# Kernel optimization log

Measured on AMD Instinct MI355X. Metric: run time of the kernel, lower is better.

## Reference

```python
import jax, jax.numpy as jnp
import numpy as np

ALPHA = 0.2  # leaky-relu negative slope AND the residual scale self.alpha

def setup_inputs() -> dict:
    key = jax.random.key(0)
    k1, k2, k3 = jax.random.split(key, 3)
    B, N, C_in, C_out = 8, 2048, 128, 128
    text = jax.random.normal(k1, (B, N, C_in), dtype=jnp.float32)
    adj = jnp.ones((B, N, N), dtype=jnp.float32)  # unused by the layer's forward
    W = jax.random.normal(k2, (C_in, C_out), dtype=jnp.float32) * (1.414 / np.sqrt(C_in + C_out))
    a = jax.random.normal(k3, (2 * C_out, 1), dtype=jnp.float32) * (1.414 / np.sqrt(2 * C_out + 1))
    return {"text": text, "adj": adj, "W": W, "a": a}

def reference(text, adj, W, a):
    # text: [B,N,C_in]; adj is unused (faithful to the source forward).
    h = jnp.einsum('bnc,cf->bnf', text, W)                  # [B,N,F]
    F_out = W.shape[1]
    a1 = a[:F_out, 0]                                       # score contribution of node i
    a2 = a[F_out:, 0]                                       # score contribution of node j
    s1 = jnp.einsum('bnf,f->bn', h, a1)                     # [B,N]
    s2 = jnp.einsum('bnf,f->bn', h, a2)                     # [B,N]
    # leakyrelu(cat(h_i,h_j) @ a) == leakyrelu(s1_i + s2_j): avoids O(N^2*2F) concat
    e = jax.nn.leaky_relu(s1[:, :, None] + s2[:, None, :], negative_slope=ALPHA)  # [B,N,N]
    attention = jax.nn.softmax(e, axis=2)                   # dropout is a no-op in eval mode
    h_prime = jnp.einsum('bij,bjf->bif', attention, h)      # [B,N,F]
    return jax.nn.elu(h_prime + ALPHA * h)
```

## Files before the change

kernel.cpp:

```cpp
#include <hip/hip_runtime.h>
#include <math.h>

#define LRELU_ALPHA 0.2f

constexpr int B_ = 8;
constexpr int N_ = 2048;
constexpr int C_ = 128;
constexpr int M_ = B_ * N_;
constexpr int SEG = 64;
constexpr int NSEG = N_ / SEG;

__global__ __launch_bounds__(512) void k_gemm(const float* __restrict__ text,
                                              const float* __restrict__ W,
                                              float* __restrict__ h) {
    __shared__ float As[64 * 33];
    __shared__ float Ws[32 * 128];
    const int tid = threadIdx.x;
    const int r0  = blockIdx.x * 64;
    const int cx  = tid & 15;
    const int ry  = tid >> 4;
    const int c0  = cx * 8;
    const int rr0 = ry * 2;

    float acc[2][8];
#pragma unroll
    for (int i = 0; i < 2; ++i)
#pragma unroll
        for (int j = 0; j < 8; ++j) acc[i][j] = 0.f;

    for (int kk = 0; kk < 128; kk += 32) {
        for (int idx = tid; idx < 64 * 32; idx += 512) {
            int r = idx >> 5, c = idx & 31;
            As[r * 33 + c] = text[(r0 + r) * 128 + kk + c];
        }
        for (int idx = tid; idx < 32 * 128; idx += 512) {
            int k = idx >> 7, f = idx & 127;
            Ws[k * 128 + f] = W[(kk + k) * 128 + f];
        }
        __syncthreads();
#pragma unroll
        for (int k = 0; k < 32; ++k) {
            float4 w0 = *(const float4*)&Ws[k * 128 + c0];
            float4 w1 = *(const float4*)&Ws[k * 128 + c0 + 4];
#pragma unroll
            for (int i = 0; i < 2; ++i) {
                float av = As[(rr0 + i) * 33 + k];
                acc[i][0] += av * w0.x; acc[i][1] += av * w0.y;
                acc[i][2] += av * w0.z; acc[i][3] += av * w0.w;
                acc[i][4] += av * w1.x; acc[i][5] += av * w1.y;
                acc[i][6] += av * w1.z; acc[i][7] += av * w1.w;
            }
        }
        __syncthreads();
    }
#pragma unroll
    for (int i = 0; i < 2; ++i) {
        int row = r0 + rr0 + i;
        float4 o0 = {acc[i][0], acc[i][1], acc[i][2], acc[i][3]};
        float4 o1 = {acc[i][4], acc[i][5], acc[i][6], acc[i][7]};
        *(float4*)&h[row * 128 + c0]     = o0;
        *(float4*)&h[row * 128 + c0 + 4] = o1;
    }
}

__global__ __launch_bounds__(256) void k_s12(const float* __restrict__ h,
                                             const float* __restrict__ a,
                                             float* __restrict__ s1,
                                             float* __restrict__ s2) {
    const int row = blockIdx.x * 4 + (threadIdx.x >> 6);
    const int t   = threadIdx.x & 63;
    float v0 = h[row * 128 + t];
    float v1 = h[row * 128 + 64 + t];
    float p1 = v0 * a[t]       + v1 * a[64 + t];
    float p2 = v0 * a[128 + t] + v1 * a[192 + t];
#pragma unroll
    for (int off = 32; off >= 1; off >>= 1) {
        p1 += __shfl_xor(p1, off);
        p2 += __shfl_xor(p2, off);
    }
    if (t == 0) { s1[row] = p1; s2[row] = p2; }
}

__global__ __launch_bounds__(1024) void k_sortscan(const float* __restrict__ s2,
                                                   float* __restrict__ s2s,
                                                   int* __restrict__ perm,
                                                   float* __restrict__ eN,
                                                   float* __restrict__ eP,
                                                   float* __restrict__ PreZ,
                                                   float* __restrict__ SufZ) {
    __shared__ float key[2048];
    __shared__ int   idxv[2048];
    __shared__ float arrN[2048];
    __shared__ float arrP[2048];
    const int b = blockIdx.x;
    const int tid = threadIdx.x;

    for (int t = tid; t < 2048; t += 1024) { key[t] = s2[b * 2048 + t]; idxv[t] = t; }
    __syncthreads();

    for (int k = 2; k <= 2048; k <<= 1) {
        for (int j = k >> 1; j > 0; j >>= 1) {
            for (int t = tid; t < 2048; t += 1024) {
                int ixj = t ^ j;
                if (ixj > t) {
                    bool up = ((t & k) == 0);
                    float ka = key[t], kb = key[ixj];
                    if ((ka > kb) == up) {
                        key[t] = kb; key[ixj] = ka;
                        int tmp = idxv[t]; idxv[t] = idxv[ixj]; idxv[ixj] = tmp;
                    }
                }
            }
            __syncthreads();
        }
    }

    for (int t = tid; t < 2048; t += 1024) {
        float kv = key[t];
        float en = expf(LRELU_ALPHA * kv);
        float ep = expf(kv);
        arrN[t] = en;
        s2s[b * 2048 + t] = kv;
        perm[b * 2048 + t] = idxv[t];
        eN[b * 2048 + t] = en;
        eP[b * 2048 + t] = ep;
    }
    __syncthreads();
    for (int t = tid; t < 2048; t += 1024) arrP[t] = expf(key[2047 - t]);
    __syncthreads();

    for (int off = 1; off < 2048; off <<= 1) {
        int t0 = tid, t1 = tid + 1024;
        float n0 = (t0 >= off) ? arrN[t0 - off] : 0.f;
        float n1 = (t1 >= off) ? arrN[t1 - off] : 0.f;
        float p0 = (t0 >= off) ? arrP[t0 - off] : 0.f;
        float p1 = (t1 >= off) ? arrP[t1 - off] : 0.f;
        __syncthreads();
        arrN[t0] += n0; arrN[t1] += n1;
        arrP[t0] += p0; arrP[t1] += p1;
        __syncthreads();
    }

    for (int t = tid; t < 2048; t += 1024) {
        PreZ[b * 2049 + t + 1] = arrN[t];
        SufZ[b * 2049 + t]     = arrP[2047 - t];
    }
    if (tid == 0) { PreZ[b * 2049] = 0.f; SufZ[b * 2049 + 2048] = 0.f; }
}

__global__ __launch_bounds__(128) void k_segsum(const float* __restrict__ h,
                                                const int* __restrict__ perm,
                                                const float* __restrict__ eN,
                                                const float* __restrict__ eP,
                                                float* __restrict__ segN,
                                                float* __restrict__ segP) {
    const int blk = blockIdx.x;
    const int b = blk >> 5, s = blk & 31;
    const int f = threadIdx.x;
    const int rbase = s * SEG;
    float an = 0.f, ap = 0.f;
    for (int r = 0; r < SEG; ++r) {
        int rr = b * 2048 + rbase + r;
        float hv = h[(b * 2048 + perm[rr]) * 128 + f];
        an += eN[rr] * hv;
        ap += eP[rr] * hv;
    }
    segN[blk * 128 + f] = an;
    segP[blk * 128 + f] = ap;
}

__global__ __launch_bounds__(128) void k_segoff(const float* __restrict__ segN,
                                                const float* __restrict__ segP,
                                                float* __restrict__ offN,
                                                float* __restrict__ offP) {
    const int b = blockIdx.x;
    const int f = threadIdx.x;
    float an = 0.f;
    for (int s = 0; s < NSEG; ++s) {
        int o = (b * NSEG + s) * 128 + f;
        offN[o] = an; an += segN[o];
    }
    float ap = 0.f;
    for (int s = NSEG - 1; s >= 0; --s) {
        int o = (b * NSEG + s) * 128 + f;
        offP[o] = ap; ap += segP[o];
    }
}

__global__ __launch_bounds__(128) void k_prefix(const float* __restrict__ h,
                                                const int* __restrict__ perm,
                                                const float* __restrict__ eN,
                                                const float* __restrict__ eP,
                                                const float* __restrict__ offN,
                                                const float* __restrict__ offP,
                                                float* __restrict__ Pre,
                                                float* __restrict__ Suf) {
    const int blk = blockIdx.x;
    const int b = blk >> 5, s = blk & 31;
    const int f = threadIdx.x;
    const int rbase = s * SEG;

    float hv[SEG];
    float an = offN[blk * 128 + f];
#pragma unroll
    for (int r = 0; r < SEG; ++r) {
        int rr = b * 2048 + rbase + r;
        hv[r] = h[(b * 2048 + perm[rr]) * 128 + f];
        Pre[(b * 2049 + rbase + r) * 128 + f] = an;
        an += eN[rr] * hv[r];
    }
    float ap = offP[blk * 128 + f];
#pragma unroll
    for (int r = SEG - 1; r >= 0; --r) {
        int rr = b * 2048 + rbase + r;
        ap += eP[rr] * hv[r];
        Suf[(b * 2049 + rbase + r) * 128 + f] = ap;
    }
    if (s == NSEG - 1) {
        Pre[(b * 2049 + 2048) * 128 + f] = an;
        Suf[(b * 2049 + 2048) * 128 + f] = 0.f;
    }
}

__global__ __launch_bounds__(256) void k_out(const float* __restrict__ h,
                                             const float* __restrict__ s1,
                                             const float* __restrict__ s2s,
                                             const float* __restrict__ PreZ,
                                             const float* __restrict__ SufZ,
                                             const float* __restrict__ Pre,
                                             const float* __restrict__ Suf,
                                             float* __restrict__ out) {
    const int tid = threadIdx.x;
    const int lr = tid >> 7, f = tid & 127;
    const int i = blockIdx.x * 2 + lr;
    const int b = i >> 11;

    const float s1v = s1[i];
    const float thr = -s1v;
    const float* keys = s2s + b * 2048;
    int lo = 0, hi = 2048;
    while (lo < hi) {
        int mid = (lo + hi) >> 1;
        if (keys[mid] <= thr) lo = mid + 1; else hi = mid;
    }
    const int r = lo;

    const float E1 = expf(s1v);
    const float E2 = expf(LRELU_ALPHA * s1v);
    const float Z  = E1 * SufZ[b * 2049 + r] + E2 * PreZ[b * 2049 + r];
    const int o = (b * 2049 + r) * 128 + f;
    const float hp = (E1 * Suf[o] + E2 * Pre[o]) / Z;
    const float hvv = h[i * 128 + f];
    const float x = hp + LRELU_ALPHA * hvv;
    out[i * 128 + f] = (x > 0.f) ? x : expm1f(x);
}

extern "C" void kernel_launch(void* const* d_in, const int* in_sizes, int n_in,
                              void* d_out, int out_size, void* d_ws, size_t ws_size,
                              hipStream_t stream) {
    const float* text = (const float*)d_in[0];
    const float* W = (const float*)d_in[2];
    const float* a = (const float*)d_in[3];
    float* out = (float*)d_out;

    float* p = (float*)d_ws;
    float* h    = p; p += (size_t)M_ * 128;
    float* s1   = p; p += M_;
    float* s2   = p; p += M_;
    float* s2s  = p; p += M_;
    int*   perm = (int*)p; p += M_;
    float* eN   = p; p += M_;
    float* eP   = p; p += M_;
    float* PreZ = p; p += B_ * 2049;
    float* SufZ = p; p += B_ * 2049;
    float* segN = p; p += B_ * NSEG * 128;
    float* segP = p; p += B_ * NSEG * 128;
    float* offN = p; p += B_ * NSEG * 128;
    float* offP = p; p += B_ * NSEG * 128;
    float* Pre  = p; p += (size_t)B_ * 2049 * 128;
    float* Suf  = p; p += (size_t)B_ * 2049 * 128;

    hipLaunchKernelGGL(k_gemm,     dim3(M_ / 64),   dim3(512),  0, stream, text, W, h);
    hipLaunchKernelGGL(k_s12,      dim3(M_ / 4),    dim3(256),  0, stream, h, a, s1, s2);
    hipLaunchKernelGGL(k_sortscan, dim3(B_),        dim3(1024), 0, stream, s2, s2s, perm, eN, eP, PreZ, SufZ);
    hipLaunchKernelGGL(k_segsum,   dim3(B_ * NSEG), dim3(128),  0, stream, h, perm, eN, eP, segN, segP);
    hipLaunchKernelGGL(k_segoff,   dim3(B_),        dim3(128),  0, stream, segN, segP, offN, offP);
    hipLaunchKernelGGL(k_prefix,   dim3(B_ * NSEG), dim3(128),  0, stream, h, perm, eN, eP, offN, offP, Pre, Suf);
    hipLaunchKernelGGL(k_out,      dim3(M_ / 2),    dim3(256),  0, stream, h, s1, s2s, PreZ, SufZ, Pre, Suf, out);
}
```

Before: 264.2 us.

## Replace bitonic sort with parallel rank counting and fuse score projection into GEMM

Fuses the s1/s2 projection and the exp computations into the GEMM epilogue. The single-block-per-batch bitonic sort and scan become a brute-force rank kernel spread over 256 blocks: each node counts how many keys are smaller to find its sorted position, and computes its threshold count and partition sums directly. This removes the binary search in the output kernel. It also halves the segment size and drops the segment-offset kernel by having each prefix block sum earlier segment totals itself. The aim is to remove the serial, low-occupancy sort stage and two kernel launches, at the cost of O(N^2) comparisons per batch and redundant offset sums.

```diff
diff --git a/kernel.cpp b/kernel.cpp
--- a/kernel.cpp
+++ b/kernel.cpp
@@ -5,14 +5,18 @@
 
 constexpr int B_ = 8;
 constexpr int N_ = 2048;
-constexpr int C_ = 128;
 constexpr int M_ = B_ * N_;
-constexpr int SEG = 64;
+constexpr int SEG = 32;
 constexpr int NSEG = N_ / SEG;
 
 __global__ __launch_bounds__(512) void k_gemm(const float* __restrict__ text,
                                               const float* __restrict__ W,
-                                              float* __restrict__ h) {
+                                              const float* __restrict__ a,
+                                              float* __restrict__ h,
+                                              float* __restrict__ s1,
+                                              float* __restrict__ s2,
+                                              float* __restrict__ eN0,
+                                              float* __restrict__ eP0) {
     __shared__ float As[64 * 33];
     __shared__ float Ws[32 * 128];
     const int tid = threadIdx.x;
@@ -53,6 +57,12 @@
         }
         __syncthreads();
     }
+
+    float4 a10 = *(const float4*)&a[c0];
+    float4 a11 = *(const float4*)&a[c0 + 4];
+    float4 a20 = *(const float4*)&a[128 + c0];
+    float4 a21 = *(const float4*)&a[128 + c0 + 4];
+
 #pragma unroll
     for (int i = 0; i < 2; ++i) {
         int row = r0 + rr0 + i;
@@ -60,160 +70,151 @@
         float4 o1 = {acc[i][4], acc[i][5], acc[i][6], acc[i][7]};
         *(float4*)&h[row * 128 + c0]     = o0;
         *(float4*)&h[row * 128 + c0 + 4] = o1;
-    }
-}
-
-__global__ __launch_bounds__(256) void k_s12(const float* __restrict__ h,
-                                             const float* __restrict__ a,
-                                             float* __restrict__ s1,
-                                             float* __restrict__ s2) {
-    const int row = blockIdx.x * 4 + (threadIdx.x >> 6);
-    const int t   = threadIdx.x & 63;
-    float v0 = h[row * 128 + t];
-    float v1 = h[row * 128 + 64 + t];
-    float p1 = v0 * a[t]       + v1 * a[64 + t];
-    float p2 = v0 * a[128 + t] + v1 * a[192 + t];
-#pragma unroll
-    for (int off = 32; off >= 1; off >>= 1) {
-        p1 += __shfl_xor(p1, off);
-        p2 += __shfl_xor(p2, off);
-    }
-    if (t == 0) { s1[row] = p1; s2[row] = p2; }
-}
-
-__global__ __launch_bounds__(1024) void k_sortscan(const float* __restrict__ s2,
-                                                   float* __restrict__ s2s,
-                                                   int* __restrict__ perm,
-                                                   float* __restrict__ eN,
-                                                   float* __restrict__ eP,
-                                                   float* __restrict__ PreZ,
-                                                   float* __restrict__ SufZ) {
-    __shared__ float key[2048];
-    __shared__ int   idxv[2048];
-    __shared__ float arrN[2048];
-    __shared__ float arrP[2048];
-    const int b = blockIdx.x;
+
+        float p1 = o0.x * a10.x + o0.y * a10.y + o0.z * a10.z + o0.w * a10.w
+                 + o1.x * a11.x + o1.y * a11.y + o1.z * a11.z + o1.w * a11.w;
+        float p2 = o0.x * a20.x + o0.y * a20.y + o0.z * a20.z + o0.w * a20.w
+                 + o1.x * a21.x + o1.y * a21.y + o1.z * a21.z + o1.w * a21.w;
+#pragma unroll
+        for (int off = 8; off >= 1; off >>= 1) {
+            p1 += __shfl_xor(p1, off);
+            p2 += __shfl_xor(p2, off);
+        }
+        if (cx == 0) {
+            s1[row] = p1;
+            s2[row] = p2;
+            eN0[row] = expf(LRELU_ALPHA * p2);
+            eP0[row] = expf(p2);
+        }
+    }
+}
+
+__global__ __launch_bounds__(512) void k_rank(const float* __restrict__ s2,
+                                              const float* __restrict__ eN0,
+                                              const float* __restrict__ eP0,
+                                              const float* __restrict__ s1,
+                                              int* __restrict__ perm,
+                                              float* __restrict__ eNs,
+                                              float* __restrict__ ePs,
+                                              int* __restrict__ rank,
+                                              float* __restrict__ ZN,
+                                              float* __restrict__ ZP) {
+    __shared__ float ls2[2048], leN[2048], leP[2048];
+    __shared__ int   redc[512], redm[512];
+    __shared__ float redn[512], redp[512];
+
+    const int b  = blockIdx.x >> 5;
+    const int eb = blockIdx.x & 31;
     const int tid = threadIdx.x;
-
-    for (int t = tid; t < 2048; t += 1024) { key[t] = s2[b * 2048 + t]; idxv[t] = t; }
+    const int e = tid & 63;
+    const int c = tid >> 6;
+
+    {
+        const float4* g2 = (const float4*)(s2  + b * 2048);
+        const float4* gn = (const float4*)(eN0 + b * 2048);
+        const float4* gp = (const float4*)(eP0 + b * 2048);
+        ((float4*)ls2)[tid] = g2[tid];
+        ((float4*)leN)[tid] = gn[tid];
+        ((float4*)leP)[tid] = gp[tid];
+    }
     __syncthreads();
 
-    for (int k = 2; k <= 2048; k <<= 1) {
-        for (int j = k >> 1; j > 0; j >>= 1) {
-            for (int t = tid; t < 2048; t += 1024) {
-                int ixj = t ^ j;
-                if (ixj > t) {
-                    bool up = ((t & k) == 0);
-                    float ka = key[t], kb = key[ixj];
-                    if ((ka > kb) == up) {
-                        key[t] = kb; key[ixj] = ka;
-                        int tmp = idxv[t]; idxv[t] = idxv[ixj]; idxv[ixj] = tmp;
-                    }
-                }
-            }
-            __syncthreads();
-        }
-    }
-
-    for (int t = tid; t < 2048; t += 1024) {
-        float kv = key[t];
-        float en = expf(LRELU_ALPHA * kv);
-        float ep = expf(kv);
-        arrN[t] = en;
-        s2s[b * 2048 + t] = kv;
-        perm[b * 2048 + t] = idxv[t];
-        eN[b * 2048 + t] = en;
-        eP[b * 2048 + t] = ep;
-    }
+    const int i  = eb * 64 + e;
+    const int gi = b * 2048 + i;
+    const float myS2 = ls2[i];
+    const float thr  = -s1[gi];
+
+    int cnt = 0, mr = 0;
+    float sn = 0.f, sp = 0.f;
+    const int j0 = c * 256;
+#pragma unroll 4
+    for (int j = j0; j < j0 + 256; j += 4) {
+        float4 v  = *(const float4*)&ls2[j];
+        float4 en = *(const float4*)&leN[j];
+        float4 ep = *(const float4*)&leP[j];
+#define PROC(vv, ee, pp, jj)                                             \
+        { bool le = (vv) <= thr;                                         \
+          cnt += le ? 1 : 0;                                             \
+          sn  += le ? (ee) : 0.f;                                        \
+          sp  += le ? 0.f : (pp);                                        \
+          mr  += ((vv) < myS2 || ((vv) == myS2 && (jj) < i)) ? 1 : 0; }
+        PROC(v.x, en.x, ep.x, j + 0)
+        PROC(v.y, en.y, ep.y, j + 1)
+        PROC(v.z, en.z, ep.z, j + 2)
+        PROC(v.w, en.w, ep.w, j + 3)
+#undef PROC
+    }
+    redc[tid] = cnt; redm[tid] = mr; redn[tid] = sn; redp[tid] = sp;
     __syncthreads();
-    for (int t = tid; t < 2048; t += 1024) arrP[t] = expf(key[2047 - t]);
-    __syncthreads();
-
-    for (int off = 1; off < 2048; off <<= 1) {
-        int t0 = tid, t1 = tid + 1024;
-        float n0 = (t0 >= off) ? arrN[t0 - off] : 0.f;
-        float n1 = (t1 >= off) ? arrN[t1 - off] : 0.f;
-        float p0 = (t0 >= off) ? arrP[t0 - off] : 0.f;
-        float p1 = (t1 >= off) ? arrP[t1 - off] : 0.f;
-        __syncthreads();
-        arrN[t0] += n0; arrN[t1] += n1;
-        arrP[t0] += p0; arrP[t1] += p1;
-        __syncthreads();
-    }
-
-    for (int t = tid; t < 2048; t += 1024) {
-        PreZ[b * 2049 + t + 1] = arrN[t];
-        SufZ[b * 2049 + t]     = arrP[2047 - t];
-    }
-    if (tid == 0) { PreZ[b * 2049] = 0.f; SufZ[b * 2049 + 2048] = 0.f; }
+    if (c == 0) {
+        int tc = 0, tm = 0; float tn = 0.f, tp = 0.f;
+#pragma unroll
+        for (int cc = 0; cc < 8; ++cc) {
+            tc += redc[cc * 64 + e];
+            tm += redm[cc * 64 + e];
+            tn += redn[cc * 64 + e];
+            tp += redp[cc * 64 + e];
+        }
+        perm[b * 2048 + tm] = i;
+        eNs [b * 2048 + tm] = leN[i];
+        ePs [b * 2048 + tm] = leP[i];
+        rank[gi] = tc;
+        ZN[gi] = tn;
+        ZP[gi] = tp;
+    }
 }
 
 __global__ __launch_bounds__(128) void k_segsum(const float* __restrict__ h,
                                                 const int* __restrict__ perm,
-                                                const float* __restrict__ eN,
-                                                const float* __restrict__ eP,
+                                                const float* __restrict__ eNs,
+                                                const float* __restrict__ ePs,
                                                 float* __restrict__ segN,
                                                 float* __restrict__ segP) {
     const int blk = blockIdx.x;
-    const int b = blk >> 5, s = blk & 31;
+    const int b = blk >> 6, s = blk & 63;
     const int f = threadIdx.x;
     const int rbase = s * SEG;
     float an = 0.f, ap = 0.f;
+#pragma unroll 4
     for (int r = 0; r < SEG; ++r) {
         int rr = b * 2048 + rbase + r;
         float hv = h[(b * 2048 + perm[rr]) * 128 + f];
-        an += eN[rr] * hv;
-        ap += eP[rr] * hv;
+        an += eNs[rr] * hv;
+        ap += ePs[rr] * hv;
     }
     segN[blk * 128 + f] = an;
     segP[blk * 128 + f] = ap;
 }
 
-__global__ __launch_bounds__(128) void k_segoff(const float* __restrict__ segN,
-                                                const float* __restrict__ segP,
-                                                float* __restrict__ offN,
-                                                float* __restrict__ offP) {
-    const int b = blockIdx.x;
-    const int f = threadIdx.x;
-    float an = 0.f;
-    for (int s = 0; s < NSEG; ++s) {
-        int o = (b * NSEG + s) * 128 + f;
-        offN[o] = an; an += segN[o];
-    }
-    float ap = 0.f;
-    for (int s = NSEG - 1; s >= 0; --s) {
-        int o = (b * NSEG + s) * 128 + f;
-        offP[o] = ap; ap += segP[o];
-    }
-}
-
 __global__ __launch_bounds__(128) void k_prefix(const float* __restrict__ h,
                                                 const int* __restrict__ perm,
-                                                const float* __restrict__ eN,
-                                                const float* __restrict__ eP,
-                                                const float* __restrict__ offN,
-                                                const float* __restrict__ offP,
+                                                const float* __restrict__ eNs,
+                                                const float* __restrict__ ePs,
+                                                const float* __restrict__ segN,
+                                                const float* __restrict__ segP,
                                                 float* __restrict__ Pre,
                                                 float* __restrict__ Suf) {
     const int blk = blockIdx.x;
-    const int b = blk >> 5, s = blk & 31;
+    const int b = blk >> 6, s = blk & 63;
     const int f = threadIdx.x;
     const int rbase = s * SEG;
 
+    float an = 0.f, ap = 0.f;
+    for (int ss = 0; ss < s; ++ss)        an += segN[(b * NSEG + ss) * 128 + f];
+    for (int ss = s + 1; ss < NSEG; ++ss) ap += segP[(b * NSEG + ss) * 128 + f];
+
     float hv[SEG];
-    float an = offN[blk * 128 + f];
 #pragma unroll
     for (int r = 0; r < SEG; ++r) {
         int rr = b * 2048 + rbase + r;
         hv[r] = h[(b * 2048 + perm[rr]) * 128 + f];
         Pre[(b * 2049 + rbase + r) * 128 + f] = an;
-        an += eN[rr] * hv[r];
-    }
-    float ap = offP[blk * 128 + f];
+        an += eNs[rr] * hv[r];
+    }
 #pragma unroll
     for (int r = SEG - 1; r >= 0; --r) {
         int rr = b * 2048 + rbase + r;
-        ap += eP[rr] * hv[r];
+        ap += ePs[rr] * hv[r];
         Suf[(b * 2049 + rbase + r) * 128 + f] = ap;
     }
     if (s == NSEG - 1) {
@@ -224,9 +225,9 @@
 
 __global__ __launch_bounds__(256) void k_out(const float* __restrict__ h,
                                              const float* __restrict__ s1,
-                                             const float* __restrict__ s2s,
-                                             const float* __restrict__ PreZ,
-                                             const float* __restrict__ SufZ,
+                                             const int* __restrict__ rank,
+                                             const float* __restrict__ ZN,
+                                             const float* __restrict__ ZP,
                                              const float* __restrict__ Pre,
                                              const float* __restrict__ Suf,
                                              float* __restrict__ out) {
@@ -236,22 +237,13 @@
     const int b = i >> 11;
 
     const float s1v = s1[i];
-    const float thr = -s1v;
-    const float* keys = s2s + b * 2048;
-    int lo = 0, hi = 2048;
-    while (lo < hi) {
-        int mid = (lo + hi) >> 1;
-        if (keys[mid] <= thr) lo = mid + 1; else hi = mid;
-    }
-    const int r = lo;
-
     const float E1 = expf(s1v);
     const float E2 = expf(LRELU_ALPHA * s1v);
-    const float Z  = E1 * SufZ[b * 2049 + r] + E2 * PreZ[b * 2049 + r];
+    const int   r  = rank[i];
+    const float Z  = E1 * ZP[i] + E2 * ZN[i];
     const int o = (b * 2049 + r) * 128 + f;
     const float hp = (E1 * Suf[o] + E2 * Pre[o]) / Z;
-    const float hvv = h[i * 128 + f];
-    const float x = hp + LRELU_ALPHA * hvv;
+    const float x = hp + LRELU_ALPHA * h[i * 128 + f];
     out[i * 128 + f] = (x > 0.f) ? x : expm1f(x);
 }
 
@@ -267,24 +259,27 @@
     float* h    = p; p += (size_t)M_ * 128;
     float* s1   = p; p += M_;
     float* s2   = p; p += M_;
-    float* s2s  = p; p += M_;
+    float* eN0  = p; p += M_;
+    float* eP0  = p; p += M_;
     int*   perm = (int*)p; p += M_;
-    float* eN   = p; p += M_;
-    float* eP   = p; p += M_;
-    float* PreZ = p; p += B_ * 2049;
-    float* SufZ = p; p += B_ * 2049;
+    float* eNs  = p; p += M_;
+    float* ePs  = p; p += M_;
+    int*   rank = (int*)p; p += M_;
+    float* ZN   = p; p += M_;
+    float* ZP   = p; p += M_;
     float* segN = p; p += B_ * NSEG * 128;
     float* segP = p; p += B_ * NSEG * 128;
-    float* offN = p; p += B_ * NSEG * 128;
-    float* offP = p; p += B_ * NSEG * 128;
     float* Pre  = p; p += (size_t)B_ * 2049 * 128;
     float* Suf  = p; p += (size_t)B_ * 2049 * 128;
 
-    hipLaunchKernelGGL(k_gemm,     dim3(M_ / 64),   dim3(512),  0, stream, text, W, h);
-    hipLaunchKernelGGL(k_s12,      dim3(M_ / 4),    dim3(256),  0, stream, h, a, s1, s2);
-    hipLaunchKernelGGL(k_sortscan, dim3(B_),        dim3(1024), 0, stream, s2, s2s, perm, eN, eP, PreZ, SufZ);
-    hipLaunchKernelGGL(k_segsum,   dim3(B_ * NSEG), dim3(128),  0, stream, h, perm, eN, eP, segN, segP);
-    hipLaunchKernelGGL(k_segoff,   dim3(B_),        dim3(128),  0, stream, segN, segP, offN, offP);
-    hipLaunchKernelGGL(k_prefix,   dim3(B_ * NSEG), dim3(128),  0, stream, h, perm, eN, eP, offN, offP, Pre, Suf);
-    hipLaunchKernelGGL(k_out,      dim3(M_ / 2),    dim3(256),  0, stream, h, s1, s2s, PreZ, SufZ, Pre, Suf, out);
-}
+    hipLaunchKernelGGL(k_gemm,   dim3(M_ / 64),   dim3(512), 0, stream,
+                       text, W, a, h, s1, s2, eN0, eP0);
+    hipLaunchKernelGGL(k_rank,   dim3(B_ * 32),   dim3(512), 0, stream,
+                       s2, eN0, eP0, s1, perm, eNs, ePs, rank, ZN, ZP);
+    hipLaunchKernelGGL(k_segsum, dim3(B_ * NSEG), dim3(128), 0, stream,
+                       h, perm, eNs, ePs, segN, segP);
+    hipLaunchKernelGGL(k_prefix, dim3(B_ * NSEG), dim3(128), 0, stream,
+                       h, perm, eNs, ePs, segN, segP, Pre, Suf);
+    hipLaunchKernelGGL(k_out,    dim3(M_ / 2),    dim3(256), 0, stream,
+                       h, s1, rank, ZN, ZP, Pre, Suf, out);
+}
```

Measured after the change: 238.8 us. 9.6% less time.
